# Kernel tuning notes

Measured on AMD Instinct MI355X. Metric: run time of the kernel, lower is better.

Reference implementation:

```python
import jax, jax.numpy as jnp
import numpy as np

D_MODEL = 1024
NUM_HEADS = 16
MAX_SEQ_LEN = 2048
BATCH = 4
SEQ_LEN = 2048


def setup_inputs() -> dict:
    key = jax.random.key(0)
    ks = jax.random.split(key, 7)
    s = 0.02
    return {
        "x": jax.random.normal(ks[0], (BATCH, SEQ_LEN, D_MODEL), dtype=jnp.float32),
        "Wq": jax.random.normal(ks[1], (D_MODEL, D_MODEL), dtype=jnp.float32) * s,
        "Wk": jax.random.normal(ks[2], (D_MODEL, D_MODEL), dtype=jnp.float32) * s,
        "Wv": jax.random.normal(ks[3], (D_MODEL, D_MODEL), dtype=jnp.float32) * s,
        "Wo": jax.random.normal(ks[4], (D_MODEL, D_MODEL), dtype=jnp.float32) * s,
        "bo": jnp.zeros((D_MODEL,), dtype=jnp.float32),
        "bias_table": jax.random.normal(ks[5], (2 * MAX_SEQ_LEN - 1, NUM_HEADS), dtype=jnp.float32) * s,
    }


def reference(x, Wq, Wk, Wv, Wo, bo, bias_table):
    B, S, D = x.shape
    H = NUM_HEADS
    hd = D // H
    scale = hd ** -0.5

    # torch Linear: y = x @ W.T
    q = (x @ Wq.T).reshape(B, S, H, hd).transpose(0, 2, 1, 3)  # [B,H,S,hd]
    k = (x @ Wk.T).reshape(B, S, H, hd).transpose(0, 2, 1, 3)
    v = (x @ Wv.T).reshape(B, S, H, hd).transpose(0, 2, 1, 3)

    scores = jnp.einsum("bhqd,bhkd->bhqk", q, k) * scale  # [B,H,S,S]

    # relative index: coords[:,None] - coords[None,:] + max_seq_len - 1
    coords = jnp.arange(S)
    rel_idx = coords[:, None] - coords[None, :] + MAX_SEQ_LEN - 1  # [S,S]
    rel_bias = bias_table[rel_idx]              # [S,S,H]
    rel_bias = rel_bias.transpose(2, 0, 1)[None]  # [1,H,S,S]

    probs = jax.nn.softmax(scores + rel_bias, axis=-1)
    ctx = jnp.einsum("bhqk,bhkd->bhqd", probs, v)  # [B,H,S,hd]
    ctx = ctx.transpose(0, 2, 1, 3).reshape(B, S, D)
    return ctx @ Wo.T + bo
```

## Files before the change

### kernel.cpp

```cpp
#include <hip/hip_runtime.h>
#include <string.h>

typedef unsigned short u16;
typedef unsigned int   u32;
typedef __attribute__((ext_vector_type(8))) short short8;
typedef __attribute__((ext_vector_type(4))) float f32x4;

__device__ __forceinline__ u16 f2b(float f) {
  u32 u = __float_as_uint(f);
  u32 r = (u + 0x7fffu + ((u >> 16) & 1u)) >> 16;
  return (u16)r;
}
__device__ __forceinline__ void cp16(const u16* g, u16* l) {
  __builtin_amdgcn_global_load_lds(
      (const __attribute__((address_space(1))) void*)g,
      (__attribute__((address_space(3))) void*)l, 16, 0, 0);
}

__global__ __launch_bounds__(256) void cvt_f2b_kernel(const float* __restrict__ in,
                                                      u16* __restrict__ out, int n) {
  int i = (blockIdx.x * 256 + threadIdx.x) * 4;
  if (i + 3 < n) {
    float4 v = *(const float4*)&in[i];
    ushort4 o = make_ushort4(f2b(v.x), f2b(v.y), f2b(v.z), f2b(v.w));
    *(ushort4*)&out[i] = o;
  }
}
__global__ __launch_bounds__(256) void cvtw_kernel(const float* __restrict__ w0,
                                                   const float* __restrict__ w1,
                                                   const float* __restrict__ w2,
                                                   const float* __restrict__ w3,
                                                   u16* __restrict__ out) {
  const float* src = (blockIdx.y == 0) ? w0 : (blockIdx.y == 1) ? w1
                   : (blockIdx.y == 2) ? w2 : w3;
  int i = (blockIdx.x * 256 + threadIdx.x) * 4;
  float4 v = *(const float4*)&src[i];
  ushort4 o = make_ushort4(f2b(v.x), f2b(v.y), f2b(v.z), f2b(v.w));
  *(ushort4*)&out[(size_t)blockIdx.y * 1048576 + i] = o;
}

template<int MODE>
__global__ __launch_bounds__(256) void gemm128_bt(
    const u16* __restrict__ A, const u16* __restrict__ Bw,
    void* __restrict__ outp, const float* __restrict__ bias,
    const int M, const int N, const int K) {
  __shared__ __attribute__((aligned(16))) u16 As[128 * 32];
  __shared__ __attribute__((aligned(16))) u16 Bs[128 * 32];

  const u16* Bw2 = Bw;
  if (MODE == 0) Bw2 += ((size_t)blockIdx.z) << 20;

  const int tid  = threadIdx.x;
  const int wave = tid >> 6, lane = tid & 63;
  const int quad = lane >> 4, l15 = lane & 15;
  const int wm   = (wave >> 1) * 64, wn = (wave & 1) * 64;
  const int m0   = blockIdx.x * 128, n0 = blockIdx.y * 128;

  const int srow = wave * 32 + (lane >> 2);
  const int scol = (lane & 3) * 8;
  const u16* gA0 = A   + (size_t)(m0 + srow) * K + scol;
  const u16* gA1 = gA0 + (size_t)16 * K;
  const u16* gB0 = Bw2 + (size_t)(n0 + srow) * K + scol;
  const u16* gB1 = gB0 + (size_t)16 * K;
  u16* lA0 = &As[(wave * 32) * 32];
  u16* lA1 = &As[(wave * 32 + 16) * 32];
  u16* lB0 = &Bs[(wave * 32) * 32];
  u16* lB1 = &Bs[(wave * 32 + 16) * 32];

  f32x4 acc[4][4] = {};
  const int nk = K >> 5;
  for (int kt = 0; kt < nk; ++kt) {
    __syncthreads();
    cp16(gA0, lA0); cp16(gA1, lA1);
    cp16(gB0, lB0); cp16(gB1, lB1);
    gA0 += 32; gA1 += 32; gB0 += 32; gB1 += 32;
    __syncthreads();
    short8 af[4], bf[4];
    #pragma unroll
    for (int mi = 0; mi < 4; ++mi)
      af[mi] = *(const short8*)&As[(wm + mi * 16 + l15) * 32 + quad * 8];
    #pragma unroll
    for (int ni = 0; ni < 4; ++ni)
      bf[ni] = *(const short8*)&Bs[(wn + ni * 16 + l15) * 32 + quad * 8];
    #pragma unroll
    for (int mi = 0; mi < 4; ++mi)
      #pragma unroll
      for (int ni = 0; ni < 4; ++ni)
        acc[mi][ni] = __builtin_amdgcn_mfma_f32_16x16x32_bf16(af[mi], bf[ni], acc[mi][ni], 0, 0, 0);
  }

  #pragma unroll
  for (int mi = 0; mi < 4; ++mi)
    #pragma unroll
    for (int ni = 0; ni < 4; ++ni) {
      if (MODE == 0 && blockIdx.z == 2) {
        int mb = m0 + wm + mi * 16 + quad * 4;
        int n  = n0 + wn + ni * 16 + l15;
        int b = mb >> 11, s = mb & 2047, h = n >> 6, d = n & 63;
        u16* out = (u16*)outp + (((size_t)2) << 23);
        ushort4 o = make_ushort4(f2b(acc[mi][ni][0]), f2b(acc[mi][ni][1]),
                                 f2b(acc[mi][ni][2]), f2b(acc[mi][ni][3]));
        *(ushort4*)&out[((((size_t)b * 16 + h) * 64 + d) << 11) + s] = o;
      } else {
        #pragma unroll
        for (int r = 0; r < 4; ++r) {
          int m = m0 + wm + mi * 16 + quad * 4 + r;
          int n = n0 + wn + ni * 16 + l15;
          float v = acc[mi][ni][r];
          if (MODE == 0) {
            int b = m >> 11, s = m & 2047, h = n >> 6, d = n & 63;
            u16* out = (u16*)outp + (((size_t)blockIdx.z) << 23);
            out[((((size_t)b * 16 + h) * 2048 + s) << 6) + d] = f2b(v);
          } else {
            ((float*)outp)[(size_t)m * N + n] = v + bias[n];
          }
        }
      }
    }
}

__global__ __launch_bounds__(256, 4) void attn_mfma_kernel(
    const u16* __restrict__ qb, const u16* __restrict__ kb, const u16* __restrict__ vtb,
    const float* __restrict__ bias_table, u16* __restrict__ ctx) {
  __shared__ __attribute__((aligned(16))) u16 Ks[64][72];
  __shared__ __attribute__((aligned(16))) u16 Vs[64][72];
  __shared__ __attribute__((aligned(16))) float bias_s[2304];

  const int tid  = threadIdx.x;
  const int wave = tid >> 6, lane = tid & 63;
  const int quad = lane >> 4, l15 = lane & 15;
  const int bh   = blockIdx.x, h = bh & 15, b = bh >> 4;
  const int q0   = blockIdx.y * 128;

  for (int i = tid; i < 2175; i += 256)
    bias_s[i] = bias_table[(q0 + i) * 16 + h] * 1.44269504f;

  short8 aQ[2][2];
  #pragma unroll
  for (int qt = 0; qt < 2; ++qt)
    #pragma unroll
    for (int ks = 0; ks < 2; ++ks)
      aQ[qt][ks] = *(const short8*)&qb[((size_t)bh * 2048 + q0 + wave * 32 + qt * 16 + l15) * 64
                                       + ks * 32 + quad * 8];

  short8 ones;
  #pragma unroll
  for (int j = 0; j < 8; ++j) ones[j] = (short)0x3F80;

  const int addrA = ((lane & 16) << 3) | (l15 << 2);
  const int addrB = addrA + 64;

  f32x4 accO[4][2] = {};
  f32x4 accL[2]    = {};

  const int srow = tid >> 2, scol = (tid & 3) * 16;

  for (int kt = 0; kt < 32; ++kt) {
    const int k0 = kt * 64;
    __syncthreads();
    {
      const u16* kp = kb  + ((size_t)bh * 2048 + k0 + srow) * 64 + scol;
      const u16* vp = vtb + (((size_t)bh * 64 + srow) << 11) + k0 + scol;
      short8 ka = *(const short8*)&kp[0];
      short8 kc = *(const short8*)&kp[8];
      short8 va = *(const short8*)&vp[0];
      short8 vc = *(const short8*)&vp[8];
      *(short8*)&Ks[srow][scol]     = ka;
      *(short8*)&Ks[srow][scol + 8] = kc;
      *(short8*)&Vs[srow][scol]     = va;
      *(short8*)&Vs[srow][scol + 8] = vc;
    }
    __syncthreads();

    short8 bK[4][2];
    #pragma unroll
    for (int nt = 0; nt < 4; ++nt)
      #pragma unroll
      for (int ks = 0; ks < 2; ++ks)
        bK[nt][ks] = *(const short8*)&Ks[nt * 16 + l15][ks * 32 + quad * 8];
    f32x4 accS[4][2] = {};
    #pragma unroll
    for (int nt = 0; nt < 4; ++nt)
      #pragma unroll
      for (int qt = 0; qt < 2; ++qt) {
        accS[nt][qt] = __builtin_amdgcn_mfma_f32_16x16x32_bf16(bK[nt][0], aQ[qt][0], accS[nt][qt], 0, 0, 0);
        accS[nt][qt] = __builtin_amdgcn_mfma_f32_16x16x32_bf16(bK[nt][1], aQ[qt][1], accS[nt][qt], 0, 0, 0);
      }

    short8 bV[4][2];
    #pragma unroll
    for (int dt = 0; dt < 4; ++dt)
      #pragma unroll
      for (int kc = 0; kc < 2; ++kc)
        bV[dt][kc] = *(const short8*)&Vs[dt * 16 + l15][kc * 32 + quad * 8];

    #pragma unroll
    for (int qt = 0; qt < 2; ++qt) {
      u32 pk[4][2];
      #pragma unroll
      for (int nt = 0; nt < 4; ++nt) {
        const int jb = wave * 32 + qt * 16 + l15 - k0 - nt * 16 - quad * 4 + 2047;
        #pragma unroll
        for (int p = 0; p < 2; ++p) {
          float e0 = __builtin_amdgcn_exp2f(fmaf(accS[nt][qt][2 * p],     0.18033688f, bias_s[jb - 2 * p]));
          float e1 = __builtin_amdgcn_exp2f(fmaf(accS[nt][qt][2 * p + 1], 0.18033688f, bias_s[jb - 2 * p - 1]));
          pk[nt][p] = (__float_as_uint(e0) >> 16) | (__float_as_uint(e1) & 0xFFFF0000u);
        }
      }
      #pragma unroll
      for (int kc = 0; kc < 2; ++kc) {
        u32 bPu[4];
        #pragma unroll
        for (int w = 0; w < 4; ++w) {
          const int ad = (w < 2) ? addrA : addrB;
          int lo = __builtin_amdgcn_ds_bpermute(ad, (int)pk[2 * kc][w & 1]);
          int hi = __builtin_amdgcn_ds_bpermute(ad, (int)pk[2 * kc + 1][w & 1]);
          bPu[w] = (lane & 32) ? (u32)hi : (u32)lo;
        }
        short8 bP;
        memcpy(&bP, bPu, 16);
        accL[qt] = __builtin_amdgcn_mfma_f32_16x16x32_bf16(ones, bP, accL[qt], 0, 0, 0);
        #pragma unroll
        for (int dt = 0; dt < 4; ++dt)
          accO[dt][qt] = __builtin_amdgcn_mfma_f32_16x16x32_bf16(bV[dt][kc], bP, accO[dt][qt], 0, 0, 0);
      }
    }
  }

  #pragma unroll
  for (int qt = 0; qt < 2; ++qt) {
    const float inv = 1.0f / accL[qt][0];
    const int q = q0 + wave * 32 + qt * 16 + l15;
    #pragma unroll
    for (int dt = 0; dt < 4; ++dt) {
      ushort4 o = make_ushort4(f2b(accO[dt][qt][0] * inv), f2b(accO[dt][qt][1] * inv),
                               f2b(accO[dt][qt][2] * inv), f2b(accO[dt][qt][3] * inv));
      *(ushort4*)&ctx[((size_t)b * 2048 + q) * 1024 + h * 64 + dt * 16 + quad * 4] = o;
    }
  }
}

extern "C" void kernel_launch(void* const* d_in, const int* in_sizes, int n_in,
                              void* d_out, int out_size, void* d_ws, size_t ws_size,
                              hipStream_t stream) {
  const float* x          = (const float*)d_in[0];
  const float* Wq         = (const float*)d_in[1];
  const float* Wk         = (const float*)d_in[2];
  const float* Wv         = (const float*)d_in[3];
  const float* Wo         = (const float*)d_in[4];
  const float* bo         = (const float*)d_in[5];
  const float* bias_table = (const float*)d_in[6];
  float* out = (float*)d_out;

  char* ws = (char*)d_ws;
  u16* xb   = (u16*)(ws);
  u16* wqb  = (u16*)(ws + 16777216);
  u16* wob  = (u16*)(ws + 16777216 + 3 * 2097152);
  u16* qb   = (u16*)(ws + 25165824);
  u16* kb   = qb + 8388608;
  u16* vtb  = kb + 8388608;
  u16* ctxb = (u16*)(ws + 75497472);

  cvt_f2b_kernel<<<8192, 256, 0, stream>>>(x, xb, 8388608);
  cvtw_kernel<<<dim3(1024, 4), 256, 0, stream>>>(Wq, Wk, Wv, Wo, wqb);

  gemm128_bt<0><<<dim3(64, 8, 3), 256, 0, stream>>>(
      xb, wqb, (void*)qb, nullptr, 8192, 1024, 1024);

  attn_mfma_kernel<<<dim3(64, 16), 256, 0, stream>>>(qb, kb, vtb, bias_table, ctxb);

  gemm128_bt<1><<<dim3(64, 8), 256, 0, stream>>>(
      ctxb, wob, (void*)out, bo, 8192, 1024, 1024);
}
```

Before: 319.7 us.

## Store V in fp16 and use f16 MFMA for PV to drop lane permutes

The V projection is now written as fp16 using packed round-toward-zero conversion. The attention kernel feeds exp'd scores straight from the QK accumulator layout into 16x16x16 f16 MFMAs, which removes the ds_bpermute shuffles and lane selects that previously rebuilt the P operand. The projection GEMM also moves from a 32-wide to a 64-wide K tile, halving the number of sync/load iterations. The trade-off is twice as many (smaller-K) MFMA instructions for PV, and fp16 probabilities that are computed without max subtraction and could overflow.

```diff
diff --git a/kernel.cpp b/kernel.cpp
--- a/kernel.cpp
+++ b/kernel.cpp
@@ -5,6 +5,8 @@
 typedef unsigned int   u32;
 typedef __attribute__((ext_vector_type(8))) short short8;
 typedef __attribute__((ext_vector_type(4))) float f32x4;
+typedef __attribute__((ext_vector_type(2))) __fp16 h2;
+typedef __attribute__((ext_vector_type(4))) __fp16 h4;
 
 __device__ __forceinline__ u16 f2b(float f) {
   u32 u = __float_as_uint(f);
@@ -44,8 +46,8 @@
     const u16* __restrict__ A, const u16* __restrict__ Bw,
     void* __restrict__ outp, const float* __restrict__ bias,
     const int M, const int N, const int K) {
-  __shared__ __attribute__((aligned(16))) u16 As[128 * 32];
-  __shared__ __attribute__((aligned(16))) u16 Bs[128 * 32];
+  __shared__ __attribute__((aligned(16))) u16 As[128 * 64];
+  __shared__ __attribute__((aligned(16))) u16 Bs[128 * 64];
 
   const u16* Bw2 = Bw;
   if (MODE == 0) Bw2 += ((size_t)blockIdx.z) << 20;
@@ -56,37 +58,44 @@
   const int wm   = (wave >> 1) * 64, wn = (wave & 1) * 64;
   const int m0   = blockIdx.x * 128, n0 = blockIdx.y * 128;
 
-  const int srow = wave * 32 + (lane >> 2);
-  const int scol = (lane & 3) * 8;
-  const u16* gA0 = A   + (size_t)(m0 + srow) * K + scol;
-  const u16* gA1 = gA0 + (size_t)16 * K;
-  const u16* gB0 = Bw2 + (size_t)(n0 + srow) * K + scol;
-  const u16* gB1 = gB0 + (size_t)16 * K;
-  u16* lA0 = &As[(wave * 32) * 32];
-  u16* lA1 = &As[(wave * 32 + 16) * 32];
-  u16* lB0 = &Bs[(wave * 32) * 32];
-  u16* lB1 = &Bs[(wave * 32 + 16) * 32];
+  const int sr8  = lane >> 3;
+  const int scol = (lane & 7) * 8;
+  const u16* gA[4]; const u16* gB[4]; u16* lA[4]; u16* lB[4];
+  #pragma unroll
+  for (int i = 0; i < 4; ++i) {
+    gA[i] = A   + (size_t)(m0 + wave * 32 + i * 8 + sr8) * K + scol;
+    gB[i] = Bw2 + (size_t)(n0 + wave * 32 + i * 8 + sr8) * K + scol;
+    lA[i] = &As[(wave * 32 + i * 8) * 64];
+    lB[i] = &Bs[(wave * 32 + i * 8) * 64];
+  }
 
   f32x4 acc[4][4] = {};
-  const int nk = K >> 5;
+  const int nk = K >> 6;
   for (int kt = 0; kt < nk; ++kt) {
     __syncthreads();
-    cp16(gA0, lA0); cp16(gA1, lA1);
-    cp16(gB0, lB0); cp16(gB1, lB1);
-    gA0 += 32; gA1 += 32; gB0 += 32; gB1 += 32;
-    __syncthreads();
-    short8 af[4], bf[4];
+    #pragma unroll
+    for (int i = 0; i < 4; ++i) { cp16(gA[i], lA[i]); cp16(gB[i], lB[i]); }
+    #pragma unroll
+    for (int i = 0; i < 4; ++i) { gA[i] += 64; gB[i] += 64; }
+    __syncthreads();
+    short8 af[4][2], bf[4][2];
     #pragma unroll
     for (int mi = 0; mi < 4; ++mi)
-      af[mi] = *(const short8*)&As[(wm + mi * 16 + l15) * 32 + quad * 8];
+      #pragma unroll
+      for (int hh = 0; hh < 2; ++hh)
+        af[mi][hh] = *(const short8*)&As[(wm + mi * 16 + l15) * 64 + hh * 32 + quad * 8];
     #pragma unroll
     for (int ni = 0; ni < 4; ++ni)
-      bf[ni] = *(const short8*)&Bs[(wn + ni * 16 + l15) * 32 + quad * 8];
-    #pragma unroll
-    for (int mi = 0; mi < 4; ++mi)
-      #pragma unroll
-      for (int ni = 0; ni < 4; ++ni)
-        acc[mi][ni] = __builtin_amdgcn_mfma_f32_16x16x32_bf16(af[mi], bf[ni], acc[mi][ni], 0, 0, 0);
+      #pragma unroll
+      for (int hh = 0; hh < 2; ++hh)
+        bf[ni][hh] = *(const short8*)&Bs[(wn + ni * 16 + l15) * 64 + hh * 32 + quad * 8];
+    #pragma unroll
+    for (int hh = 0; hh < 2; ++hh)
+      #pragma unroll
+      for (int mi = 0; mi < 4; ++mi)
+        #pragma unroll
+        for (int ni = 0; ni < 4; ++ni)
+          acc[mi][ni] = __builtin_amdgcn_mfma_f32_16x16x32_bf16(af[mi][hh], bf[ni][hh], acc[mi][ni], 0, 0, 0);
   }
 
   #pragma unroll
@@ -98,8 +107,11 @@
         int n  = n0 + wn + ni * 16 + l15;
         int b = mb >> 11, s = mb & 2047, h = n >> 6, d = n & 63;
         u16* out = (u16*)outp + (((size_t)2) << 23);
-        ushort4 o = make_ushort4(f2b(acc[mi][ni][0]), f2b(acc[mi][ni][1]),
-                                 f2b(acc[mi][ni][2]), f2b(acc[mi][ni][3]));
+        h2 p0 = __builtin_amdgcn_cvt_pkrtz(acc[mi][ni][0], acc[mi][ni][1]);
+        h2 p1 = __builtin_amdgcn_cvt_pkrtz(acc[mi][ni][2], acc[mi][ni][3]);
+        ushort4 o;
+        memcpy(&o.x, &p0, 4);
+        memcpy(&o.z, &p1, 4);
         *(ushort4*)&out[((((size_t)b * 16 + h) * 64 + d) << 11) + s] = o;
       } else {
         #pragma unroll
@@ -143,12 +155,7 @@
       aQ[qt][ks] = *(const short8*)&qb[((size_t)bh * 2048 + q0 + wave * 32 + qt * 16 + l15) * 64
                                        + ks * 32 + quad * 8];
 
-  short8 ones;
-  #pragma unroll
-  for (int j = 0; j < 8; ++j) ones[j] = (short)0x3F80;
-
-  const int addrA = ((lane & 16) << 3) | (l15 << 2);
-  const int addrB = addrA + 64;
+  const h4 onesh = {(__fp16)1.f, (__fp16)1.f, (__fp16)1.f, (__fp16)1.f};
 
   f32x4 accO[4][2] = {};
   f32x4 accL[2]    = {};
@@ -187,42 +194,32 @@
         accS[nt][qt] = __builtin_amdgcn_mfma_f32_16x16x32_bf16(bK[nt][1], aQ[qt][1], accS[nt][qt], 0, 0, 0);
       }
 
-    short8 bV[4][2];
-    #pragma unroll
-    for (int dt = 0; dt < 4; ++dt)
-      #pragma unroll
-      for (int kc = 0; kc < 2; ++kc)
-        bV[dt][kc] = *(const short8*)&Vs[dt * 16 + l15][kc * 32 + quad * 8];
+    h4 aV[4][4];
+    #pragma unroll
+    for (int nt = 0; nt < 4; ++nt)
+      #pragma unroll
+      for (int dt = 0; dt < 4; ++dt)
+        aV[nt][dt] = *(const h4*)&Vs[dt * 16 + l15][nt * 16 + quad * 4];
 
     #pragma unroll
     for (int qt = 0; qt < 2; ++qt) {
-      u32 pk[4][2];
       #pragma unroll
       for (int nt = 0; nt < 4; ++nt) {
-        const int jb = wave * 32 + qt * 16 + l15 - k0 - nt * 16 - quad * 4 + 2047;
-        #pragma unroll
-        for (int p = 0; p < 2; ++p) {
-          float e0 = __builtin_amdgcn_exp2f(fmaf(accS[nt][qt][2 * p],     0.18033688f, bias_s[jb - 2 * p]));
-          float e1 = __builtin_amdgcn_exp2f(fmaf(accS[nt][qt][2 * p + 1], 0.18033688f, bias_s[jb - 2 * p - 1]));
-          pk[nt][p] = (__float_as_uint(e0) >> 16) | (__float_as_uint(e1) & 0xFFFF0000u);
-        }
-      }
-      #pragma unroll
-      for (int kc = 0; kc < 2; ++kc) {
-        u32 bPu[4];
-        #pragma unroll
-        for (int w = 0; w < 4; ++w) {
-          const int ad = (w < 2) ? addrA : addrB;
-          int lo = __builtin_amdgcn_ds_bpermute(ad, (int)pk[2 * kc][w & 1]);
-          int hi = __builtin_amdgcn_ds_bpermute(ad, (int)pk[2 * kc + 1][w & 1]);
-          bPu[w] = (lane & 32) ? (u32)hi : (u32)lo;
-        }
-        short8 bP;
-        memcpy(&bP, bPu, 16);
-        accL[qt] = __builtin_amdgcn_mfma_f32_16x16x32_bf16(ones, bP, accL[qt], 0, 0, 0);
+        const int jbm = (wave * 32 + qt * 16 + l15) - (nt * 16 + quad * 4) - k0 + 2044;
+        float bb0 = bias_s[jbm],     bb1 = bias_s[jbm + 1];
+        float bb2 = bias_s[jbm + 2], bb3 = bias_s[jbm + 3];
+        float p0 = __builtin_amdgcn_exp2f(fmaf(accS[nt][qt][0], 0.18033688f, bb3));
+        float p1 = __builtin_amdgcn_exp2f(fmaf(accS[nt][qt][1], 0.18033688f, bb2));
+        float p2 = __builtin_amdgcn_exp2f(fmaf(accS[nt][qt][2], 0.18033688f, bb1));
+        float p3 = __builtin_amdgcn_exp2f(fmaf(accS[nt][qt][3], 0.18033688f, bb0));
+        h2 e01 = __builtin_amdgcn_cvt_pkrtz(p0, p1);
+        h2 e23 = __builtin_amdgcn_cvt_pkrtz(p2, p3);
+        h4 bP;
+        bP[0] = e01[0]; bP[1] = e01[1]; bP[2] = e23[0]; bP[3] = e23[1];
+        accL[qt] = __builtin_amdgcn_mfma_f32_16x16x16f16(onesh, bP, accL[qt], 0, 0, 0);
         #pragma unroll
         for (int dt = 0; dt < 4; ++dt)
-          accO[dt][qt] = __builtin_amdgcn_mfma_f32_16x16x32_bf16(bV[dt][kc], bP, accO[dt][qt], 0, 0, 0);
+          accO[dt][qt] = __builtin_amdgcn_mfma_f32_16x16x16f16(aV[nt][dt], bP, accO[dt][qt], 0, 0, 0);
       }
     }
   }
```

Measured after the change: 316.4 us. No clear change (-1.0%).

## Double-buffer K via async LDS loads, switch PV to fp16 MFMA without bpermute

Applied to the files above, without the earlier changes.

K tiles are now loaded straight into a double-buffered, XOR-swizzled LDS area with global_load_lds for the next tile, and V is prefetched into registers a tile ahead. This overlaps global loads with compute. The P·V product now uses fp16 16x16x16 MFMAs whose operand layout matches the score accumulator, so the ds_bpermute shuffles go away. The V projection output is written as fp16 to match. In exchange, softmax probabilities and V lose range compared with bf16, and the PV MFMA instruction count doubles.

```diff
diff --git a/kernel.cpp b/kernel.cpp
--- a/kernel.cpp
+++ b/kernel.cpp
@@ -5,6 +5,8 @@
 typedef unsigned int   u32;
 typedef __attribute__((ext_vector_type(8))) short short8;
 typedef __attribute__((ext_vector_type(4))) float f32x4;
+typedef __attribute__((ext_vector_type(2))) __fp16 h2;
+typedef __attribute__((ext_vector_type(4))) __fp16 h4;
 
 __device__ __forceinline__ u16 f2b(float f) {
   u32 u = __float_as_uint(f);
@@ -98,8 +100,11 @@
         int n  = n0 + wn + ni * 16 + l15;
         int b = mb >> 11, s = mb & 2047, h = n >> 6, d = n & 63;
         u16* out = (u16*)outp + (((size_t)2) << 23);
-        ushort4 o = make_ushort4(f2b(acc[mi][ni][0]), f2b(acc[mi][ni][1]),
-                                 f2b(acc[mi][ni][2]), f2b(acc[mi][ni][3]));
+        h2 p0 = __builtin_amdgcn_cvt_pkrtz(acc[mi][ni][0], acc[mi][ni][1]);
+        h2 p1 = __builtin_amdgcn_cvt_pkrtz(acc[mi][ni][2], acc[mi][ni][3]);
+        ushort4 o;
+        memcpy(&o.x, &p0, 4);
+        memcpy(&o.z, &p1, 4);
         *(ushort4*)&out[((((size_t)b * 16 + h) * 64 + d) << 11) + s] = o;
       } else {
         #pragma unroll
@@ -122,7 +127,7 @@
 __global__ __launch_bounds__(256, 4) void attn_mfma_kernel(
     const u16* __restrict__ qb, const u16* __restrict__ kb, const u16* __restrict__ vtb,
     const float* __restrict__ bias_table, u16* __restrict__ ctx) {
-  __shared__ __attribute__((aligned(16))) u16 Ks[64][72];
+  __shared__ __attribute__((aligned(16))) u16 Ks[2][64 * 64];
   __shared__ __attribute__((aligned(16))) u16 Vs[64][72];
   __shared__ __attribute__((aligned(16))) float bias_s[2304];
 
@@ -143,41 +148,58 @@
       aQ[qt][ks] = *(const short8*)&qb[((size_t)bh * 2048 + q0 + wave * 32 + qt * 16 + l15) * 64
                                        + ks * 32 + quad * 8];
 
-  short8 ones;
-  #pragma unroll
-  for (int j = 0; j < 8; ++j) ones[j] = (short)0x3F80;
-
-  const int addrA = ((lane & 16) << 3) | (l15 << 2);
-  const int addrB = addrA + 64;
+  const h4 onesh = {(__fp16)1.f, (__fp16)1.f, (__fp16)1.f, (__fp16)1.f};
 
   f32x4 accO[4][2] = {};
   f32x4 accL[2]    = {};
 
-  const int srow = tid >> 2, scol = (tid & 3) * 16;
+  const int krow = lane >> 3;
+  const int kchk = (lane & 7) ^ krow;
+  const u16* kbase = kb + (((size_t)bh * 2048) << 6);
+  const int xsw = l15 & 7;
+
+  const int srow = tid >> 2, t0 = tid & 3;
+  const u16* vrow = vtb + (((size_t)bh * 64 + srow) << 11) + t0 * 16;
+
+  short8 vpre0 = *(const short8*)&vrow[0];
+  short8 vpre1 = *(const short8*)&vrow[8];
+  #pragma unroll
+  for (int g = 0; g < 2; ++g)
+    cp16(kbase + (size_t)(wave * 16 + g * 8 + krow) * 64 + kchk * 8,
+         &Ks[0][(wave * 16 + g * 8) * 64]);
 
   for (int kt = 0; kt < 32; ++kt) {
+    const int cur = kt & 1;
+    __syncthreads();
+    {
+      ushort4 w0, w1, w2, w3;
+      memcpy(&w0, &vpre0, 8);  memcpy(&w1, ((const char*)&vpre0) + 8, 8);
+      memcpy(&w2, &vpre1, 8);  memcpy(&w3, ((const char*)&vpre1) + 8, 8);
+      *(ushort4*)&Vs[srow][ 0 + t0 * 4] = w0;
+      *(ushort4*)&Vs[srow][16 + t0 * 4] = w1;
+      *(ushort4*)&Vs[srow][32 + t0 * 4] = w2;
+      *(ushort4*)&Vs[srow][48 + t0 * 4] = w3;
+    }
+    __syncthreads();
+    if (kt < 31) {
+      const u16* vp = vrow + ((kt + 1) << 6);
+      vpre0 = *(const short8*)&vp[0];
+      vpre1 = *(const short8*)&vp[8];
+      #pragma unroll
+      for (int g = 0; g < 2; ++g)
+        cp16(kbase + (size_t)((kt + 1) * 64 + wave * 16 + g * 8 + krow) * 64 + kchk * 8,
+             &Ks[1 - cur][(wave * 16 + g * 8) * 64]);
+    }
+
     const int k0 = kt * 64;
-    __syncthreads();
-    {
-      const u16* kp = kb  + ((size_t)bh * 2048 + k0 + srow) * 64 + scol;
-      const u16* vp = vtb + (((size_t)bh * 64 + srow) << 11) + k0 + scol;
-      short8 ka = *(const short8*)&kp[0];
-      short8 kc = *(const short8*)&kp[8];
-      short8 va = *(const short8*)&vp[0];
-      short8 vc = *(const short8*)&vp[8];
-      *(short8*)&Ks[srow][scol]     = ka;
-      *(short8*)&Ks[srow][scol + 8] = kc;
-      *(short8*)&Vs[srow][scol]     = va;
-      *(short8*)&Vs[srow][scol + 8] = vc;
-    }
-    __syncthreads();
 
     short8 bK[4][2];
     #pragma unroll
     for (int nt = 0; nt < 4; ++nt)
       #pragma unroll
       for (int ks = 0; ks < 2; ++ks)
-        bK[nt][ks] = *(const short8*)&Ks[nt * 16 + l15][ks * 32 + quad * 8];
+        bK[nt][ks] = *(const short8*)&Ks[cur][(nt * 16 + l15) * 64
+                                             + (((ks * 4 + quad) ^ xsw) << 3)];
     f32x4 accS[4][2] = {};
     #pragma unroll
     for (int nt = 0; nt < 4; ++nt)
@@ -187,43 +209,38 @@
         accS[nt][qt] = __builtin_amdgcn_mfma_f32_16x16x32_bf16(bK[nt][1], aQ[qt][1], accS[nt][qt], 0, 0, 0);
       }
 
-    short8 bV[4][2];
-    #pragma unroll
-    for (int dt = 0; dt < 4; ++dt)
-      #pragma unroll
-      for (int kc = 0; kc < 2; ++kc)
-        bV[dt][kc] = *(const short8*)&Vs[dt * 16 + l15][kc * 32 + quad * 8];
-
-    #pragma unroll
-    for (int qt = 0; qt < 2; ++qt) {
-      u32 pk[4][2];
+    h4 bP[2][4];
+    #pragma unroll
+    for (int qt = 0; qt < 2; ++qt)
       #pragma unroll
       for (int nt = 0; nt < 4; ++nt) {
-        const int jb = wave * 32 + qt * 16 + l15 - k0 - nt * 16 - quad * 4 + 2047;
+        const int jbm = (wave * 32 + qt * 16 + l15) - (nt * 16 + quad * 4) - k0 + 2044;
+        float bb0 = bias_s[jbm],     bb1 = bias_s[jbm + 1];
+        float bb2 = bias_s[jbm + 2], bb3 = bias_s[jbm + 3];
+        float p0 = __builtin_amdgcn_exp2f(fmaf(accS[nt][qt][0], 0.18033688f, bb3));
+        float p1 = __builtin_amdgcn_exp2f(fmaf(accS[nt][qt][1], 0.18033688f, bb2));
+        float p2 = __builtin_amdgcn_exp2f(fmaf(accS[nt][qt][2], 0.18033688f, bb1));
+        float p3 = __builtin_amdgcn_exp2f(fmaf(accS[nt][qt][3], 0.18033688f, bb0));
+        h2 e01 = __builtin_amdgcn_cvt_pkrtz(p0, p1);
+        h2 e23 = __builtin_amdgcn_cvt_pkrtz(p2, p3);
+        h4 bp;
+        bp[0] = e01[0]; bp[1] = e01[1]; bp[2] = e23[0]; bp[3] = e23[1];
+        bP[qt][nt] = bp;
+        accL[qt] = __builtin_amdgcn_mfma_f32_16x16x16f16(onesh, bp, accL[qt], 0, 0, 0);
+      }
+
+    #pragma unroll
+    for (int dt = 0; dt < 4; ++dt) {
+      short8 v0 = *(const short8*)&Vs[dt * 16 + l15][quad * 16];
+      short8 v1 = *(const short8*)&Vs[dt * 16 + l15][quad * 16 + 8];
+      h4 aV[4];
+      memcpy(&aV[0], &v0, 8);  memcpy(&aV[1], ((const char*)&v0) + 8, 8);
+      memcpy(&aV[2], &v1, 8);  memcpy(&aV[3], ((const char*)&v1) + 8, 8);
+      #pragma unroll
+      for (int qt = 0; qt < 2; ++qt)
         #pragma unroll
-        for (int p = 0; p < 2; ++p) {
-          float e0 = __builtin_amdgcn_exp2f(fmaf(accS[nt][qt][2 * p],     0.18033688f, bias_s[jb - 2 * p]));
-          float e1 = __builtin_amdgcn_exp2f(fmaf(accS[nt][qt][2 * p + 1], 0.18033688f, bias_s[jb - 2 * p - 1]));
-          pk[nt][p] = (__float_as_uint(e0) >> 16) | (__float_as_uint(e1) & 0xFFFF0000u);
-        }
-      }
-      #pragma unroll
-      for (int kc = 0; kc < 2; ++kc) {
-        u32 bPu[4];
-        #pragma unroll
-        for (int w = 0; w < 4; ++w) {
-          const int ad = (w < 2) ? addrA : addrB;
-          int lo = __builtin_amdgcn_ds_bpermute(ad, (int)pk[2 * kc][w & 1]);
-          int hi = __builtin_amdgcn_ds_bpermute(ad, (int)pk[2 * kc + 1][w & 1]);
-          bPu[w] = (lane & 32) ? (u32)hi : (u32)lo;
-        }
-        short8 bP;
-        memcpy(&bP, bPu, 16);
-        accL[qt] = __builtin_amdgcn_mfma_f32_16x16x32_bf16(ones, bP, accL[qt], 0, 0, 0);
-        #pragma unroll
-        for (int dt = 0; dt < 4; ++dt)
-          accO[dt][qt] = __builtin_amdgcn_mfma_f32_16x16x32_bf16(bV[dt][kc], bP, accO[dt][qt], 0, 0, 0);
-      }
+        for (int nt = 0; nt < 4; ++nt)
+          accO[dt][qt] = __builtin_amdgcn_mfma_f32_16x16x16f16(aV[nt], bP[qt][nt], accO[dt][qt], 0, 0, 0);
     }
   }
 
```

After: 295.4 us. 7.6% less time.
